# Performance work log

Measured on AMD Instinct MI355X. Metric: run time of the kernel, lower is better.

## Reference

```python
import jax, jax.numpy as jnp
import numpy as np

ETA = 0.01   # nudging rate from __init__ default
EPS = 1e-8   # cosine-similarity epsilon


def setup_inputs() -> dict:
    key = jax.random.key(0)
    ks = jax.random.split(key, 6)
    B, F, S, E, D = 64, 512, 8192, 500000, 1024
    return {
        "heatmap_features_batch": jax.random.normal(ks[0], (B, F), dtype=jnp.float32),
        "grad_output_batch": jax.random.normal(ks[1], (B, F), dtype=jnp.float32),
        "sign_features": jax.random.normal(ks[2], (S, F), dtype=jnp.float32),
        "edge_weight": jax.random.uniform(ks[3], (E,), dtype=jnp.float32),
        "edge_disease": jax.random.randint(ks[4], (E,), 0, D, dtype=jnp.int32),
        "edge_sign": jax.random.randint(ks[5], (E,), 0, S, dtype=jnp.int32),
        "num_diseases": D,
    }


def reference(heatmap_features_batch, grad_output_batch, sign_features,
              edge_weight, edge_disease, edge_sign, num_diseases):
    # Cosine similarity between every sample's heatmap feature vector and every
    # sign node's stored feature vector, rescaled to [0, 1].
    Hn = heatmap_features_batch / (
        jnp.linalg.norm(heatmap_features_batch, axis=1, keepdims=True) + EPS)
    Sn = sign_features / (
        jnp.linalg.norm(sign_features, axis=1, keepdims=True) + EPS)
    sim = (jnp.einsum('bf,sf->bs', Hn, Sn) + 1.0) * 0.5          # [B, S]

    # Per-edge weighted similarity, gathered at each edge's sign node.
    contrib = sim[:, edge_sign] * edge_weight[None, :]           # [B, E]

    # Scatter-add edge contributions into the disease (source) index.
    agg = jax.ops.segment_sum(contrib.T, edge_disease,
                              num_segments=num_diseases)         # [D, B]

    # Per-sample gradient norm factor g^(i) = ||grad_i||_2.
    gnorm = jnp.linalg.norm(grad_output_batch, axis=1)           # [B]

    return ETA * gnorm[:, None] * agg.T                          # [B, D]
```

## Files before the change

kernel.cpp:

```cpp
#include <hip/hip_runtime.h>
#include <math.h>

#define EPS 1e-8f
#define SCB 256
#define NG1 128
#define CAP 768

typedef __attribute__((ext_vector_type(8))) __bf16 bf16x8;
typedef __attribute__((ext_vector_type(4))) float f32x4;

__device__ __forceinline__ unsigned short f2bf(float x) {
    unsigned int u = __float_as_uint(x);
    u += 0x7FFFu + ((u >> 16) & 1u);
    return (unsigned short)(u >> 16);
}
__device__ __forceinline__ unsigned int pack2(float lo, float hi) {
    return (unsigned int)f2bf(lo) | ((unsigned int)f2bf(hi) << 16);
}

__global__ __launch_bounds__(256) void k_norms(
        const float* __restrict__ Sg, const float* __restrict__ Hg,
        const float* __restrict__ Gg, unsigned short* __restrict__ Sgb,
        unsigned short* __restrict__ Hsb, float* __restrict__ gscale,
        int* __restrict__ cursor, int Srows, int Fdim, int Bdim, int Dd) {
    int bid = blockIdx.x;
    int tid = threadIdx.x;
    int lane = tid & 63, w = tid >> 6;
    int ns4 = Srows >> 2;

    if (bid < ns4) {
        int s = bid * 4 + w;
        const float4* p = (const float4*)(Sg + (size_t)s * Fdim);
        float4 a = p[2 * lane], c = p[2 * lane + 1];
        float acc = a.x * a.x + a.y * a.y + a.z * a.z + a.w * a.w
                  + c.x * c.x + c.y * c.y + c.z * c.z + c.w * c.w;
        #pragma unroll
        for (int off = 32; off; off >>= 1) acc += __shfl_xor(acc, off, 64);
        float rv = 1.0f / (sqrtf(acc) + EPS);
        uint4 o;
        o.x = pack2(a.x * rv, a.y * rv);
        o.y = pack2(a.z * rv, a.w * rv);
        o.z = pack2(c.x * rv, c.y * rv);
        o.w = pack2(c.z * rv, c.w * rv);
        *(uint4*)(Sgb + (size_t)s * Fdim + lane * 8) = o;
    } else if (bid < ns4 + (Bdim >> 2)) {
        int b = (bid - ns4) * 4 + w;
        const float4* ph = (const float4*)(Hg + (size_t)b * Fdim);
        const float4* pg = (const float4*)(Gg + (size_t)b * Fdim);
        float4 h0 = ph[2 * lane], h1 = ph[2 * lane + 1];
        float4 g0 = pg[2 * lane], g1 = pg[2 * lane + 1];
        float ah = h0.x * h0.x + h0.y * h0.y + h0.z * h0.z + h0.w * h0.w
                 + h1.x * h1.x + h1.y * h1.y + h1.z * h1.z + h1.w * h1.w;
        float ag = g0.x * g0.x + g0.y * g0.y + g0.z * g0.z + g0.w * g0.w
                 + g1.x * g1.x + g1.y * g1.y + g1.z * g1.z + g1.w * g1.w;
        #pragma unroll
        for (int off = 32; off; off >>= 1) {
            ah += __shfl_xor(ah, off, 64);
            ag += __shfl_xor(ag, off, 64);
        }
        float hn = 1.0f / (sqrtf(ah) + EPS);
        if (lane == 0) gscale[b] = 0.005f * sqrtf(ag);
        uint4 o;
        o.x = pack2(h0.x * hn, h0.y * hn);
        o.y = pack2(h0.z * hn, h0.w * hn);
        o.z = pack2(h1.x * hn, h1.y * hn);
        o.w = pack2(h1.z * hn, h1.w * hn);
        *(uint4*)(Hsb + (size_t)b * Fdim + lane * 8) = o;
    } else {
        for (int i = tid; i < Dd; i += 256) cursor[i] = 0;
    }
}

__global__ __launch_bounds__(256) void k_g1scat(
        const unsigned short* __restrict__ Sgb,
        const unsigned short* __restrict__ Hsb, float* __restrict__ Pt,
        const int* __restrict__ ed, const int* __restrict__ es,
        const float* __restrict__ ew, int* __restrict__ cursor,
        int2* __restrict__ sorted, int Srows, int Fdim, int E, int Dd) {
    __shared__ int cnt[1024];
    int id = blockIdx.x;
    int tid = threadIdx.x;

    if (id < NG1) {
        int lane = tid & 63, w = tid >> 6;
        int r16 = lane & 15, q = lane >> 4;
        int s0 = (id * 4 + w) * 16;
        const bf16x8* Ap = (const bf16x8*)(Sgb + (size_t)(s0 + r16) * Fdim) + q;
        const bf16x8* Bp = (const bf16x8*)(Hsb + (size_t)r16 * Fdim) + q;

        f32x4 acc0 = {0.f, 0.f, 0.f, 0.f};
        f32x4 acc1 = {0.f, 0.f, 0.f, 0.f};
        f32x4 acc2 = {0.f, 0.f, 0.f, 0.f};
        f32x4 acc3 = {0.f, 0.f, 0.f, 0.f};

        #pragma unroll 4
        for (int kt = 0; kt < 16; kt++) {
            bf16x8 a  = Ap[kt * 4];
            bf16x8 b0 = Bp[kt * 4];
            bf16x8 b1 = Bp[kt * 4 + 16 * 64];
            bf16x8 b2 = Bp[kt * 4 + 32 * 64];
            bf16x8 b3 = Bp[kt * 4 + 48 * 64];
            acc0 = __builtin_amdgcn_mfma_f32_16x16x32_bf16(a, b0, acc0, 0, 0, 0);
            acc1 = __builtin_amdgcn_mfma_f32_16x16x32_bf16(a, b1, acc1, 0, 0, 0);
            acc2 = __builtin_amdgcn_mfma_f32_16x16x32_bf16(a, b2, acc2, 0, 0, 0);
            acc3 = __builtin_amdgcn_mfma_f32_16x16x32_bf16(a, b3, acc3, 0, 0, 0);
        }
        #pragma unroll
        for (int r = 0; r < 4; r++) {
            int s = s0 + q * 4 + r;
            float* row = Pt + (size_t)s * 64 + r16;
            row[0]  = acc0[r];
            row[16] = acc1[r];
            row[32] = acc2[r];
            row[48] = acc3[r];
        }
    } else {
        int h = id - NG1;
        for (int i = tid; i < Dd; i += 256) cnt[i] = 0;
        __syncthreads();
        int chunk = (E + SCB - 1) / SCB;
        int e0 = h * chunk;
        int e1 = min(E, e0 + chunk);
        int myd[8], mys[8], myr[8];
        float myw[8];
        #pragma unroll
        for (int i = 0; i < 8; i++) {
            int e = e0 + tid + i * 256;
            myd[i] = -1;
            if (e < e1) {
                myd[i] = ed[e]; mys[i] = es[e]; myw[i] = ew[e];
                myr[i] = atomicAdd(&cnt[myd[i]], 1);
            }
        }
        __syncthreads();
        for (int d = tid; d < Dd; d += 256) {
            int c = cnt[d];
            if (c) cnt[d] = atomicAdd(&cursor[d], c);
        }
        __syncthreads();
        #pragma unroll
        for (int i = 0; i < 8; i++) {
            if (myd[i] >= 0) {
                int pos = cnt[myd[i]] + myr[i];
                sorted[(size_t)myd[i] * CAP + pos] =
                    make_int2(mys[i], __float_as_int(myw[i]));
            }
        }
    }
}

__global__ __launch_bounds__(256) void k_gather(
        const int2* __restrict__ sorted, const float* __restrict__ Pt,
        const int* __restrict__ cursor, const float* __restrict__ gscale,
        float* __restrict__ out, int Dd) {
    __shared__ float sacc[4][64];
    __shared__ float scs[4];
    int d = blockIdx.x;
    int tid = threadIdx.x;
    int lane = tid & 63, w = tid >> 6;
    int cnt = cursor[d];
    const int2* sp = sorted + (size_t)d * CAP;
    float acc = 0.f, cs = 0.f;
    #pragma unroll 8
    for (int i = w; i < cnt; i += 4) {
        int2 p = sp[i];
        float wt = __int_as_float(p.y);
        acc += wt * Pt[(size_t)p.x * 64 + lane];
        cs += wt;
    }
    sacc[w][lane] = acc;
    if (lane == 0) scs[w] = cs;
    __syncthreads();
    if (tid < 64) {
        float a = sacc[0][tid] + sacc[1][tid] + sacc[2][tid] + sacc[3][tid]
                + scs[0] + scs[1] + scs[2] + scs[3];
        out[(size_t)tid * Dd + d] = gscale[tid] * a;
    }
}

extern "C" void kernel_launch(void* const* d_in, const int* in_sizes, int n_in,
                              void* d_out, int out_size, void* d_ws, size_t ws_size,
                              hipStream_t stream) {
    const float* H  = (const float*)d_in[0];
    const float* G  = (const float*)d_in[1];
    const float* Sg = (const float*)d_in[2];
    const float* ew = (const float*)d_in[3];
    const int*   ed = (const int*)d_in[4];
    const int*   es = (const int*)d_in[5];

    const int B = 64;
    const int F = in_sizes[0] / B;
    const int S = in_sizes[2] / F;
    const int E = in_sizes[3];
    const int D = out_size / B;
    float* out = (float*)d_out;

    float* ws = (float*)d_ws;
    size_t off = 0;
    unsigned short* Sgb = (unsigned short*)(ws + off); off += (size_t)S * F / 2;
    unsigned short* Hsb = (unsigned short*)(ws + off); off += (size_t)B * F / 2;
    float* gscale = ws + off; off += 256;
    float* Pt     = ws + off; off += (size_t)S * B;
    int*   cursor = (int*)(ws + off); off += (size_t)D;
    int2*  sorted = (int2*)(ws + off); off += 2 * (size_t)D * CAP;

    k_norms<<<S / 4 + B / 4 + 1, 256, 0, stream>>>(Sg, H, G, Sgb, Hsb, gscale,
                                                   cursor, S, F, B, D);
    k_g1scat<<<NG1 + SCB, 256, 0, stream>>>(Sgb, Hsb, Pt, ed, es, ew,
                                            cursor, sorted, S, F, E, D);
    k_gather<<<D, 256, 0, stream>>>(sorted, Pt, cursor, gscale, out, D);
}
```

Measured before the change: 118.2 us.

## Store normalized bf16 operands in MFMA fragment order for coalesced loads

The norm kernel now handles 16 rows per block and writes the bf16-normalized S and H matrices in a tiled layout that matches the MFMA 16x16x32 operand fragment order. Each lane of the GEMM can then load its fragment with a fully contiguous 16-byte-per-lane access. The GEMM preloads all 16 A fragments and software-pipelines the B loads one k-step ahead. This targets strided, poorly coalesced fragment loads, at the cost of more registers per thread and a block-level shared-memory reduction in the norm kernel.

```diff
diff --git a/kernel.cpp b/kernel.cpp
--- a/kernel.cpp
+++ b/kernel.cpp
@@ -23,49 +23,61 @@
         const float* __restrict__ Gg, unsigned short* __restrict__ Sgb,
         unsigned short* __restrict__ Hsb, float* __restrict__ gscale,
         int* __restrict__ cursor, int Srows, int Fdim, int Bdim, int Dd) {
+    __shared__ float redA[4][17];
+    __shared__ float redB[4][17];
     int bid = blockIdx.x;
     int tid = threadIdx.x;
-    int lane = tid & 63, w = tid >> 6;
-    int ns4 = Srows >> 2;
-
-    if (bid < ns4) {
-        int s = bid * 4 + w;
-        const float4* p = (const float4*)(Sg + (size_t)s * Fdim);
-        float4 a = p[2 * lane], c = p[2 * lane + 1];
-        float acc = a.x * a.x + a.y * a.y + a.z * a.z + a.w * a.w
-                  + c.x * c.x + c.y * c.y + c.z * c.z + c.w * c.w;
-        #pragma unroll
-        for (int off = 32; off; off >>= 1) acc += __shfl_xor(acc, off, 64);
-        float rv = 1.0f / (sqrtf(acc) + EPS);
-        uint4 o;
-        o.x = pack2(a.x * rv, a.y * rv);
-        o.y = pack2(a.z * rv, a.w * rv);
-        o.z = pack2(c.x * rv, c.y * rv);
-        o.w = pack2(c.z * rv, c.w * rv);
-        *(uint4*)(Sgb + (size_t)s * Fdim + lane * 8) = o;
-    } else if (bid < ns4 + (Bdim >> 2)) {
-        int b = (bid - ns4) * 4 + w;
-        const float4* ph = (const float4*)(Hg + (size_t)b * Fdim);
-        const float4* pg = (const float4*)(Gg + (size_t)b * Fdim);
-        float4 h0 = ph[2 * lane], h1 = ph[2 * lane + 1];
-        float4 g0 = pg[2 * lane], g1 = pg[2 * lane + 1];
-        float ah = h0.x * h0.x + h0.y * h0.y + h0.z * h0.z + h0.w * h0.w
-                 + h1.x * h1.x + h1.y * h1.y + h1.z * h1.z + h1.w * h1.w;
-        float ag = g0.x * g0.x + g0.y * g0.y + g0.z * g0.z + g0.w * g0.w
-                 + g1.x * g1.x + g1.y * g1.y + g1.z * g1.z + g1.w * g1.w;
-        #pragma unroll
-        for (int off = 32; off; off >>= 1) {
-            ah += __shfl_xor(ah, off, 64);
-            ag += __shfl_xor(ag, off, 64);
-        }
-        float hn = 1.0f / (sqrtf(ah) + EPS);
-        if (lane == 0) gscale[b] = 0.005f * sqrtf(ag);
-        uint4 o;
-        o.x = pack2(h0.x * hn, h0.y * hn);
-        o.y = pack2(h0.z * hn, h0.w * hn);
-        o.z = pack2(h1.x * hn, h1.y * hn);
-        o.w = pack2(h1.z * hn, h1.w * hn);
-        *(uint4*)(Hsb + (size_t)b * Fdim + lane * 8) = o;
+    int lane = tid & 63, wv = tid >> 6;
+    int r = tid & 15, cg = tid >> 4;
+    int nsT = Srows >> 4;
+
+    if (bid < nsT + (Bdim >> 4)) {
+        bool isH = bid >= nsT;
+        int t = isH ? bid - nsT : bid;
+        const float* basep = isH ? Hg : Sg;
+        const float4* src = (const float4*)(basep + ((size_t)t * 16 + r) * Fdim);
+
+        float4 v[8];
+        float ss = 0.f, sgq = 0.f;
+        #pragma unroll
+        for (int g = 0; g < 4; g++) {
+            int c = cg + g * 16;
+            float4 x = src[c * 2], y = src[c * 2 + 1];
+            v[2 * g] = x; v[2 * g + 1] = y;
+            ss += x.x * x.x + x.y * x.y + x.z * x.z + x.w * x.w
+                + y.x * y.x + y.y * y.y + y.z * y.z + y.w * y.w;
+        }
+        if (isH) {
+            const float4* srcg = (const float4*)(Gg + ((size_t)t * 16 + r) * Fdim);
+            #pragma unroll
+            for (int g = 0; g < 4; g++) {
+                int c = cg + g * 16;
+                float4 x = srcg[c * 2], y = srcg[c * 2 + 1];
+                sgq += x.x * x.x + x.y * x.y + x.z * x.z + x.w * x.w
+                     + y.x * y.x + y.y * y.y + y.z * y.z + y.w * y.w;
+            }
+        }
+        ss  += __shfl_xor(ss, 16, 64);  ss  += __shfl_xor(ss, 32, 64);
+        sgq += __shfl_xor(sgq, 16, 64); sgq += __shfl_xor(sgq, 32, 64);
+        if (lane < 16) { redA[wv][lane] = ss; redB[wv][lane] = sgq; }
+        __syncthreads();
+        float tot = redA[0][r] + redA[1][r] + redA[2][r] + redA[3][r];
+        float rv = 1.0f / (sqrtf(tot) + EPS);
+        if (isH && tid < 16) {
+            float tg = redB[0][tid] + redB[1][tid] + redB[2][tid] + redB[3][tid];
+            gscale[t * 16 + tid] = 0.005f * sqrtf(tg);
+        }
+        uint4* dp = (uint4*)(isH ? Hsb : Sgb);
+        #pragma unroll
+        for (int g = 0; g < 4; g++) {
+            int c = cg + g * 16;
+            uint4 o;
+            o.x = pack2(v[2 * g].x * rv,     v[2 * g].y * rv);
+            o.y = pack2(v[2 * g].z * rv,     v[2 * g].w * rv);
+            o.z = pack2(v[2 * g + 1].x * rv, v[2 * g + 1].y * rv);
+            o.w = pack2(v[2 * g + 1].z * rv, v[2 * g + 1].w * rv);
+            dp[(size_t)t * 1024 + (size_t)c * 16 + r] = o;
+        }
     } else {
         for (int i = tid; i < Dd; i += 256) cursor[i] = 0;
     }
@@ -83,36 +95,43 @@
 
     if (id < NG1) {
         int lane = tid & 63, w = tid >> 6;
-        int r16 = lane & 15, q = lane >> 4;
-        int s0 = (id * 4 + w) * 16;
-        const bf16x8* Ap = (const bf16x8*)(Sgb + (size_t)(s0 + r16) * Fdim) + q;
-        const bf16x8* Bp = (const bf16x8*)(Hsb + (size_t)r16 * Fdim) + q;
+        int wt = id * 4 + w;
+        const bf16x8* A  = (const bf16x8*)Sgb + (size_t)wt * 1024 + lane;
+        const bf16x8* Bp = (const bf16x8*)Hsb + lane;
+
+        bf16x8 a[16];
+        #pragma unroll
+        for (int kt = 0; kt < 16; kt++) a[kt] = A[kt * 64];
 
         f32x4 acc0 = {0.f, 0.f, 0.f, 0.f};
         f32x4 acc1 = {0.f, 0.f, 0.f, 0.f};
         f32x4 acc2 = {0.f, 0.f, 0.f, 0.f};
         f32x4 acc3 = {0.f, 0.f, 0.f, 0.f};
 
-        #pragma unroll 4
+        bf16x8 b0 = Bp[0], b1 = Bp[1024], b2 = Bp[2048], b3 = Bp[3072];
+        #pragma unroll
         for (int kt = 0; kt < 16; kt++) {
-            bf16x8 a  = Ap[kt * 4];
-            bf16x8 b0 = Bp[kt * 4];
-            bf16x8 b1 = Bp[kt * 4 + 16 * 64];
-            bf16x8 b2 = Bp[kt * 4 + 32 * 64];
-            bf16x8 b3 = Bp[kt * 4 + 48 * 64];
-            acc0 = __builtin_amdgcn_mfma_f32_16x16x32_bf16(a, b0, acc0, 0, 0, 0);
-            acc1 = __builtin_amdgcn_mfma_f32_16x16x32_bf16(a, b1, acc1, 0, 0, 0);
-            acc2 = __builtin_amdgcn_mfma_f32_16x16x32_bf16(a, b2, acc2, 0, 0, 0);
-            acc3 = __builtin_amdgcn_mfma_f32_16x16x32_bf16(a, b3, acc3, 0, 0, 0);
-        }
-        #pragma unroll
-        for (int r = 0; r < 4; r++) {
-            int s = s0 + q * 4 + r;
+            bf16x8 c0 = b0, c1 = b1, c2 = b2, c3 = b3;
+            if (kt < 15) {
+                int o = (kt + 1) * 64;
+                b0 = Bp[o];        b1 = Bp[o + 1024];
+                b2 = Bp[o + 2048]; b3 = Bp[o + 3072];
+            }
+            acc0 = __builtin_amdgcn_mfma_f32_16x16x32_bf16(a[kt], c0, acc0, 0, 0, 0);
+            acc1 = __builtin_amdgcn_mfma_f32_16x16x32_bf16(a[kt], c1, acc1, 0, 0, 0);
+            acc2 = __builtin_amdgcn_mfma_f32_16x16x32_bf16(a[kt], c2, acc2, 0, 0, 0);
+            acc3 = __builtin_amdgcn_mfma_f32_16x16x32_bf16(a[kt], c3, acc3, 0, 0, 0);
+        }
+        int r16 = lane & 15, q = lane >> 4;
+        int s0 = wt * 16;
+        #pragma unroll
+        for (int rr = 0; rr < 4; rr++) {
+            int s = s0 + q * 4 + rr;
             float* row = Pt + (size_t)s * 64 + r16;
-            row[0]  = acc0[r];
-            row[16] = acc1[r];
-            row[32] = acc2[r];
-            row[48] = acc3[r];
+            row[0]  = acc0[rr];
+            row[16] = acc1[rr];
+            row[32] = acc2[rr];
+            row[48] = acc3[rr];
         }
     } else {
         int h = id - NG1;
@@ -204,8 +223,8 @@
     int*   cursor = (int*)(ws + off); off += (size_t)D;
     int2*  sorted = (int2*)(ws + off); off += 2 * (size_t)D * CAP;
 
-    k_norms<<<S / 4 + B / 4 + 1, 256, 0, stream>>>(Sg, H, G, Sgb, Hsb, gscale,
-                                                   cursor, S, F, B, D);
+    k_norms<<<S / 16 + B / 16 + 1, 256, 0, stream>>>(Sg, H, G, Sgb, Hsb, gscale,
+                                                     cursor, S, F, B, D);
     k_g1scat<<<NG1 + SCB, 256, 0, stream>>>(Sgb, Hsb, Pt, ed, es, ew,
                                             cursor, sorted, S, F, E, D);
     k_gather<<<D, 256, 0, stream>>>(sorted, Pt, cursor, gscale, out, D);
```

After: 119.8 us. About the same (+1.3%).
